# Optimization experiments

Hardware: AMD Instinct MI355X
Metric: run time of the kernel (lower is better)

The kernel has to match this reference:

```python
import jax, jax.numpy as jnp
import numpy as np

N, B, T, D = 4, 4, 512, 512
H, DK, DV = 8, 64, 64
LN_EPS = 1e-5


def setup_inputs() -> dict:
    key = jax.random.key(0)
    ks = jax.random.split(key, 5)
    s = 1.0 / np.sqrt(D)
    return {
        "x": jax.random.normal(ks[0], (N, B, T, D), jnp.float32),
        "Wq": jax.random.normal(ks[1], (D, H * DK), jnp.float32) * s,
        "bq": jnp.zeros((H * DK,), jnp.float32),
        "Wk": jax.random.normal(ks[2], (D, H * DK), jnp.float32) * s,
        "bk": jnp.zeros((H * DK,), jnp.float32),
        "Wv": jax.random.normal(ks[3], (D, H * DV), jnp.float32) * s,
        "bv": jnp.zeros((H * DV,), jnp.float32),
        "Wo": jax.random.normal(ks[4], (H * DV, D), jnp.float32) * (1.0 / np.sqrt(H * DV)),
        "bo": jnp.zeros((D,), jnp.float32),
        "gamma": jnp.ones((D,), jnp.float32),
        "beta": jnp.zeros((D,), jnp.float32),
    }


def reference(x, Wq, bq, Wk, bk, Wv, bv, Wo, bo, gamma, beta):
    # x: [N, B, T, D] -- N variables, each [B, T, D]
    n = x.shape[0]
    # Project once per variable (the torch code redundantly recomputes K/V per query var).
    q = (x @ Wq + bq).reshape(n, B, T, H, DK).transpose(0, 1, 3, 2, 4)  # [N,B,H,T,DK]
    k = (x @ Wk + bk).reshape(n, B, T, H, DK).transpose(0, 1, 3, 2, 4)  # [N,B,H,T,DK]
    v = (x @ Wv + bv).reshape(n, B, T, H, DV).transpose(0, 1, 3, 2, 4)  # [N,B,H,T,DV]
    # All-pairs attention: softmax over keys of EACH key-variable separately.
    scores = jnp.einsum('qbhtk,cbhsk->qcbhts', q, k) / np.sqrt(DK)  # [Nq,Nc,B,H,T,T]
    attn = jax.nn.softmax(scores, axis=-1)
    ctx = jnp.einsum('qcbhts,cbhsv->qcbhtv', attn, v)  # [Nq,Nc,B,H,T,DV]
    ctx = ctx.transpose(0, 1, 2, 4, 3, 5).reshape(n, n, B, T, H * DV)
    out = ctx @ Wo + bo                     # per-pair output projection
    out = out.sum(axis=1) / n               # average over key variables -> [N,B,T,D]
    res = x + out
    mu = res.mean(axis=-1, keepdims=True)
    var = res.var(axis=-1, keepdims=True)
    y = (res - mu) / jnp.sqrt(var + LN_EPS) * gamma + beta
    return y
```

## Files before the change

kernel.cpp:

```cpp
#include <hip/hip_runtime.h>


typedef __bf16 bf16x8 __attribute__((ext_vector_type(8)));
typedef __bf16 bf16x4 __attribute__((ext_vector_type(4)));
typedef short shortx4 __attribute__((ext_vector_type(4)));
typedef float floatx4 __attribute__((ext_vector_type(4)));
typedef float floatx16 __attribute__((ext_vector_type(16)));
typedef unsigned short ushortx8 __attribute__((ext_vector_type(8)));

static __device__ __forceinline__ unsigned short f2bf(float f) {
  union { __bf16 h; unsigned short u; } c; c.h = (__bf16)f; return c.u;
}

__global__ __launch_bounds__(256) void cvt_f32_bf16(
    const float* __restrict__ in, unsigned short* __restrict__ out)
{
  const int i = blockIdx.x * 256 + threadIdx.x;
  const float4 a = ((const float4*)in)[i * 2];
  const float4 b = ((const float4*)in)[i * 2 + 1];
  ushortx8 o;
  o[0] = f2bf(a.x); o[1] = f2bf(a.y); o[2] = f2bf(a.z); o[3] = f2bf(a.w);
  o[4] = f2bf(b.x); o[5] = f2bf(b.y); o[6] = f2bf(b.z); o[7] = f2bf(b.w);
  *(ushortx8*)(out + (size_t)i * 8) = o;
}

__global__ __launch_bounds__(256) void transpose_w(
    const float* __restrict__ W0, const float* __restrict__ W1,
    const float* __restrict__ W2, const float* __restrict__ W3,
    unsigned short* __restrict__ T0, unsigned short* __restrict__ T1,
    unsigned short* __restrict__ T2, unsigned short* __restrict__ T3)
{
  __shared__ unsigned short lds[64][65];
  const float* W; unsigned short* T;
  if (blockIdx.z == 0)      { W = W0; T = T0; }
  else if (blockIdx.z == 1) { W = W1; T = T1; }
  else if (blockIdx.z == 2) { W = W2; T = T2; }
  else                      { W = W3; T = T3; }
  const int xx = threadIdx.x;
  const int yy = threadIdx.y;
  const int k0 = blockIdx.x * 64, n0 = blockIdx.y * 64;
#pragma unroll
  for (int i = 0; i < 16; ++i) {
    const int row = yy * 16 + i;
    lds[row][xx] = f2bf(W[(size_t)(k0 + row) * 512 + n0 + xx]);
  }
  __syncthreads();
#pragma unroll
  for (int i = 0; i < 16; ++i) {
    const int nr = yy * 16 + i;
    T[(size_t)(n0 + nr) * 512 + k0 + xx] = lds[xx][nr];
  }
}

template<int MODE>
__global__ __launch_bounds__(256) void gemm64(
    const unsigned short* __restrict__ A,
    const unsigned short* __restrict__ BT,
    const float* __restrict__ bias,
    void* __restrict__ Cout, float scale)
{
  __shared__ __align__(16) unsigned short lA[64][72];
  __shared__ __align__(16) unsigned short lB[64][72];
  const int tid  = threadIdx.x;
  const int wv   = tid >> 6, lane = tid & 63;
  const int quad = lane >> 4, l16 = lane & 15;
  const int m0 = blockIdx.x * 64, n0 = blockIdx.y * 64;
  floatx4 acc[4] = {};
  const int lrow = tid >> 2, lc0 = (tid & 3) * 16;

  for (int kc = 0; kc < 512; kc += 64) {
    __syncthreads();
    const unsigned short* as = A + (size_t)(m0 + lrow) * 512 + kc + lc0;
    *(bf16x8*)&lA[lrow][lc0]     = *(const bf16x8*)as;
    *(bf16x8*)&lA[lrow][lc0 + 8] = *(const bf16x8*)(as + 8);
    const unsigned short* bs = BT + (size_t)(n0 + lrow) * 512 + kc + lc0;
    *(bf16x8*)&lB[lrow][lc0]     = *(const bf16x8*)bs;
    *(bf16x8*)&lB[lrow][lc0 + 8] = *(const bf16x8*)(bs + 8);
    __syncthreads();
    bf16x8 a0 = *(const bf16x8*)&lA[wv * 16 + l16][quad * 8];
    bf16x8 a1 = *(const bf16x8*)&lA[wv * 16 + l16][32 + quad * 8];
#pragma unroll
    for (int ni = 0; ni < 4; ++ni) {
      bf16x8 b0 = *(const bf16x8*)&lB[ni * 16 + l16][quad * 8];
      bf16x8 b1 = *(const bf16x8*)&lB[ni * 16 + l16][32 + quad * 8];
      acc[ni] = __builtin_amdgcn_mfma_f32_16x16x32_bf16(a0, b0, acc[ni], 0, 0, 0);
      acc[ni] = __builtin_amdgcn_mfma_f32_16x16x32_bf16(a1, b1, acc[ni], 0, 0, 0);
    }
  }

  const int mbase = m0 + wv * 16 + quad * 4;
  float bv4[4];
  if (MODE != 2) {
#pragma unroll
    for (int ni = 0; ni < 4; ++ni) bv4[ni] = bias[n0 + ni * 16 + l16];
  }
#pragma unroll
  for (int ni = 0; ni < 4; ++ni) {
    const int n = n0 + ni * 16 + l16;
#pragma unroll
    for (int r = 0; r < 4; ++r) {
      const int m = mbase + r;
      float v = acc[ni][r];
      if (MODE != 2) v = (v + bv4[ni]) * scale;
      if (MODE == 0) {
        const int nb = m >> 9, t = m & 511, hh = n >> 6, dk = n & 63;
        ((unsigned short*)Cout)[((size_t)(nb * 8 + hh) * 512 + t) * 64 + dk] = f2bf(v);
      } else if (MODE == 1) {
        const int nb = m >> 9, t = m & 511, hh = n >> 6, dk = n & 63;
        ((unsigned short*)Cout)[((size_t)(nb * 8 + hh) * 64 + dk) * 512 + t] = f2bf(v);
      } else {
        ((float*)Cout)[(size_t)m * 512 + n] = v;
      }
    }
  }
}

__global__ __launch_bounds__(256) void flash_kernel(
    const unsigned short* __restrict__ Q,
    const unsigned short* __restrict__ K,
    const unsigned short* __restrict__ VT,
    unsigned short* __restrict__ CTX)
{
  __shared__ __align__(16) unsigned short lK[2][64][72];
  __shared__ __align__(16) unsigned short lV[2][64][68];
  const int tid  = threadIdx.x;
  const int wv   = tid >> 6, lane = tid & 63;
  const int l32  = lane & 31, u = lane >> 5;

  const int lin  = blockIdx.y * 4 + blockIdx.x;
  const int xcd  = lin & 7, slot = lin >> 3;
  const int nbh  = xcd * 16 + (slot >> 2);
  const int t0   = (slot & 3) * 128;
  const int h = nbh & 7, nb = nbh >> 3, b = nb & 3;

  const unsigned short* qbase = Q + ((size_t)nbh * 512 + (t0 + wv * 32 + l32)) * 64;
  bf16x8 qf[4];
#pragma unroll
  for (int c16 = 0; c16 < 4; ++c16)
    qf[c16] = *(const bf16x8*)(qbase + c16 * 16 + u * 8);

  const int srow = tid >> 2, sc0 = (tid & 3) * 16;
  const unsigned short *kptr, *vptr;
  auto setptr = [&](int it) {
    const int c = it >> 3, s0 = (it & 7) * 64;
    const size_t kvbh = (size_t)((c * 4 + b) * 8 + h);
    kptr = K  + kvbh * (512 * 64) + (size_t)(s0 + srow) * 64 + sc0;
    vptr = VT + kvbh * (64 * 512) + (size_t)srow * 512 + s0 + sc0;
  };
  bf16x8 rk0, rk1, rv0, rv1;
  auto loadregs = [&]() {
    rk0 = *(const bf16x8*)kptr; rk1 = *(const bf16x8*)(kptr + 8);
    rv0 = *(const bf16x8*)vptr; rv1 = *(const bf16x8*)(vptr + 8);
  };
  auto writebuf = [&](int p) {
    *(bf16x8*)&lK[p][srow][sc0]     = rk0;
    *(bf16x8*)&lK[p][srow][sc0 + 8] = rk1;
    union { bf16x8 v8; bf16x4 v4[2]; } c0, c1;
    c0.v8 = rv0; c1.v8 = rv1;
    *(bf16x4*)&lV[p][srow][sc0]      = c0.v4[0];
    *(bf16x4*)&lV[p][srow][sc0 + 4]  = c0.v4[1];
    *(bf16x4*)&lV[p][srow][sc0 + 8]  = c1.v4[0];
    *(bf16x4*)&lV[p][srow][sc0 + 12] = c1.v4[1];
  };

  setptr(0); loadregs();
  writebuf(0);
  setptr(1); loadregs();
  __syncthreads();

  floatx16 ofin0 = {}, ofin1 = {};
  floatx16 oc0, oc1;
  float lacc;

  for (int it = 0; it < 32; ++it) {
    const int cur = it & 1;
    const int st = it & 7;
    if (st == 0) { oc0 = floatx16{}; oc1 = floatx16{}; lacc = 0.f; }

    if (it < 31) writebuf(cur ^ 1);
    if (it < 30) { setptr(it + 2); loadregs(); }

    floatx16 sacc0 = {}, sacc1 = {};
#pragma unroll
    for (int c16 = 0; c16 < 4; ++c16) {
      bf16x8 ak0 = *(const bf16x8*)&lK[cur][l32][c16 * 16 + u * 8];
      bf16x8 ak1 = *(const bf16x8*)&lK[cur][32 + l32][c16 * 16 + u * 8];
      sacc0 = __builtin_amdgcn_mfma_f32_32x32x16_bf16(ak0, qf[c16], sacc0, 0, 0, 0);
      sacc1 = __builtin_amdgcn_mfma_f32_32x32x16_bf16(ak1, qf[c16], sacc1, 0, 0, 0);
    }

#pragma unroll
    for (int sb = 0; sb < 2; ++sb) {
      const floatx16& sa = sb ? sacc1 : sacc0;
#pragma unroll
      for (int c8 = 0; c8 < 4; ++c8) {
        float e0 = __expf(sa[4 * c8 + 0] - 12.0f);
        float e1 = __expf(sa[4 * c8 + 1] - 12.0f);
        float e2 = __expf(sa[4 * c8 + 2] - 12.0f);
        float e3 = __expf(sa[4 * c8 + 3] - 12.0f);
        lacc += (e0 + e1) + (e2 + e3);
        shortx4 pf;
        pf[0] = (short)f2bf(e0); pf[1] = (short)f2bf(e1);
        pf[2] = (short)f2bf(e2); pf[3] = (short)f2bf(e3);
        const int sloc = sb * 32 + c8 * 8 + u * 4;
        shortx4 vf0 = *(const shortx4*)&lV[cur][l32][sloc];
        shortx4 vf1 = *(const shortx4*)&lV[cur][32 + l32][sloc];
        oc0 = __builtin_amdgcn_mfma_f32_32x32x8bf16_1k(pf, vf0, oc0, 0, 0, 0);
        oc1 = __builtin_amdgcn_mfma_f32_32x32x8bf16_1k(pf, vf1, oc1, 0, 0, 0);
      }
    }

    if (st == 7) {
      float s = lacc;
      s += __shfl_xor(s, 32);
      const float inv = 1.0f / s;
#pragma unroll
      for (int r = 0; r < 16; ++r) {
        const int trow = (r & 3) + 8 * (r >> 2) + 4 * u;
        const float invr = __shfl(inv, trow);
        ofin0[r] += oc0[r] * invr;
        ofin1[r] += oc1[r] * invr;
      }
    }
    __syncthreads();
  }

  const int mbase = nb * 512 + t0 + wv * 32;
#pragma unroll
  for (int r = 0; r < 16; ++r) {
    const int trow = (r & 3) + 8 * (r >> 2) + 4 * u;
    const size_t rowoff = (size_t)(mbase + trow) * 512 + h * 64;
    CTX[rowoff + l32]      = f2bf(ofin0[r]);
    CTX[rowoff + 32 + l32] = f2bf(ofin1[r]);
  }
}

__global__ __launch_bounds__(256) void ln_kernel(
    const float* __restrict__ x, const float* __restrict__ tmp,
    const float* __restrict__ bo, const float* __restrict__ gamma,
    const float* __restrict__ beta, float* __restrict__ out)
{
  const int row = blockIdx.x;
  const int t = threadIdx.x;
  const size_t base = (size_t)row * 512;
  const float r0 = x[base + t]       + 0.25f * tmp[base + t]       + bo[t];
  const float r1 = x[base + t + 256] + 0.25f * tmp[base + t + 256] + bo[t + 256];
  float s = r0 + r1, sq = r0 * r0 + r1 * r1;
#pragma unroll
  for (int off = 1; off < 64; off <<= 1) {
    s  += __shfl_xor(s, off);
    sq += __shfl_xor(sq, off);
  }
  __shared__ float ls[4], lq[4];
  const int wv = t >> 6, lane = t & 63;
  if (lane == 0) { ls[wv] = s; lq[wv] = sq; }
  __syncthreads();
  s  = ls[0] + ls[1] + ls[2] + ls[3];
  sq = lq[0] + lq[1] + lq[2] + lq[3];
  const float mu  = s * (1.0f / 512.0f);
  const float var = sq * (1.0f / 512.0f) - mu * mu;
  const float inv = rsqrtf(var + 1e-5f);
  out[base + t]       = (r0 - mu) * inv * gamma[t]       + beta[t];
  out[base + t + 256] = (r1 - mu) * inv * gamma[t + 256] + beta[t + 256];
}

extern "C" void kernel_launch(void* const* d_in, const int* in_sizes, int n_in,
                              void* d_out, int out_size, void* d_ws, size_t ws_size,
                              hipStream_t stream) {
  const float* x     = (const float*)d_in[0];
  const float* Wq    = (const float*)d_in[1];
  const float* bq    = (const float*)d_in[2];
  const float* Wk    = (const float*)d_in[3];
  const float* bk    = (const float*)d_in[4];
  const float* Wv    = (const float*)d_in[5];
  const float* bv    = (const float*)d_in[6];
  const float* Wo    = (const float*)d_in[7];
  const float* bo    = (const float*)d_in[8];
  const float* gamma = (const float*)d_in[9];
  const float* beta  = (const float*)d_in[10];
  float* out = (float*)d_out;

  char* w = (char*)d_ws;
  unsigned short* x_bf  = (unsigned short*)(w);
  unsigned short* q_bf  = (unsigned short*)(w + (size_t)8  * 1024 * 1024);
  unsigned short* k_bf  = (unsigned short*)(w + (size_t)16 * 1024 * 1024);
  unsigned short* vt_bf = (unsigned short*)(w + (size_t)24 * 1024 * 1024);
  unsigned short* ctx   = (unsigned short*)(w + (size_t)32 * 1024 * 1024);
  unsigned short* wqT   = (unsigned short*)(w + (size_t)40 * 1024 * 1024);
  unsigned short* wkT   = wqT + 262144;
  unsigned short* wvT   = wkT + 262144;
  unsigned short* woT   = wvT + 262144;
  float* tmp            = (float*)(w);

  cvt_f32_bf16<<<2048, 256, 0, stream>>>(x, x_bf);
  transpose_w<<<dim3(8, 8, 4), dim3(64, 4), 0, stream>>>(Wq, Wk, Wv, Wo, wqT, wkT, wvT, woT);
  gemm64<0><<<dim3(128, 8), 256, 0, stream>>>(x_bf, wqT, bq, q_bf, 0.125f);
  gemm64<0><<<dim3(128, 8), 256, 0, stream>>>(x_bf, wkT, bk, k_bf, 1.0f);
  gemm64<1><<<dim3(128, 8), 256, 0, stream>>>(x_bf, wvT, bv, vt_bf, 1.0f);
  flash_kernel<<<dim3(4, 128), 256, 0, stream>>>(q_bf, k_bf, vt_bf, ctx);
  gemm64<2><<<dim3(128, 8), 256, 0, stream>>>(ctx, woT, nullptr, tmp, 1.0f);
  ln_kernel<<<8192, 256, 0, stream>>>(x, tmp, bo, gamma, beta, out);
}
```

Baseline: 204.8 us.

## Split attention over key-variable groups, fuse QKV GEMMs and input conversion

The flash kernel now splits the four key variables into two groups, which doubles the number of blocks. Each group writes a partial context, and a new reduce kernel sums the two. The separate fp32-to-bf16 conversion of x is folded into a single merged QKV GEMM launch that covers all three projections. The softmax moves to exp2, with the log2(e) factor folded into the Q scale and the constant shift used to initialise the score accumulators. In exchange, this adds an extra bf16 partial-sum round trip through memory and an extra kernel launch.

Measured after the change: 214.3 us. 1.05x slower.

```diff
diff --git a/kernel.cpp b/kernel.cpp
--- a/kernel.cpp
+++ b/kernel.cpp
@@ -11,18 +11,12 @@
 static __device__ __forceinline__ unsigned short f2bf(float f) {
   union { __bf16 h; unsigned short u; } c; c.h = (__bf16)f; return c.u;
 }
-
-__global__ __launch_bounds__(256) void cvt_f32_bf16(
-    const float* __restrict__ in, unsigned short* __restrict__ out)
-{
-  const int i = blockIdx.x * 256 + threadIdx.x;
-  const float4 a = ((const float4*)in)[i * 2];
-  const float4 b = ((const float4*)in)[i * 2 + 1];
-  ushortx8 o;
-  o[0] = f2bf(a.x); o[1] = f2bf(a.y); o[2] = f2bf(a.z); o[3] = f2bf(a.w);
-  o[4] = f2bf(b.x); o[5] = f2bf(b.y); o[6] = f2bf(b.z); o[7] = f2bf(b.w);
-  *(ushortx8*)(out + (size_t)i * 8) = o;
-}
+static __device__ __forceinline__ float bf2f(unsigned short u) {
+  union { unsigned u32; float f; } c; c.u32 = ((unsigned)u) << 16; return c.f;
+}
+
+#define QSCALE 0.18033688011112042f
+#define SHIFT2 (-17.312340489609306f)
 
 __global__ __launch_bounds__(256) void transpose_w(
     const float* __restrict__ W0, const float* __restrict__ W1,
@@ -52,12 +46,78 @@
   }
 }
 
-template<int MODE>
-__global__ __launch_bounds__(256) void gemm64(
+__global__ __launch_bounds__(256) void gemm_qkv(
+    const float* __restrict__ X,
+    const unsigned short* __restrict__ BT,
+    const float* __restrict__ bq, const float* __restrict__ bk,
+    const float* __restrict__ bv,
+    unsigned short* __restrict__ Qo, unsigned short* __restrict__ Ko,
+    unsigned short* __restrict__ Vo)
+{
+  __shared__ __align__(16) unsigned short lA[64][72];
+  __shared__ __align__(16) unsigned short lB[64][72];
+  const int tid  = threadIdx.x;
+  const int wv   = tid >> 6, lane = tid & 63;
+  const int quad = lane >> 4, l16 = lane & 15;
+  const int m0 = blockIdx.x * 64, n0g = blockIdx.y * 64;
+  const int sel = n0g >> 9;
+  const int n0  = n0g & 511;
+  const float* bias = (sel == 0) ? bq : (sel == 1) ? bk : bv;
+  unsigned short* outp = (sel == 0) ? Qo : (sel == 1) ? Ko : Vo;
+  const float scale = (sel == 0) ? QSCALE : 1.0f;
+  floatx4 acc[4] = {};
+  const int lrow = tid >> 2, lc0 = (tid & 3) * 16;
+
+  for (int kc = 0; kc < 512; kc += 64) {
+    __syncthreads();
+    const float* as = X + (size_t)(m0 + lrow) * 512 + kc + lc0;
+    float4 a0 = *(const float4*)as,       a1 = *(const float4*)(as + 4);
+    float4 a2 = *(const float4*)(as + 8), a3 = *(const float4*)(as + 12);
+    ushortx8 p0, p1;
+    p0[0]=f2bf(a0.x); p0[1]=f2bf(a0.y); p0[2]=f2bf(a0.z); p0[3]=f2bf(a0.w);
+    p0[4]=f2bf(a1.x); p0[5]=f2bf(a1.y); p0[6]=f2bf(a1.z); p0[7]=f2bf(a1.w);
+    p1[0]=f2bf(a2.x); p1[1]=f2bf(a2.y); p1[2]=f2bf(a2.z); p1[3]=f2bf(a2.w);
+    p1[4]=f2bf(a3.x); p1[5]=f2bf(a3.y); p1[6]=f2bf(a3.z); p1[7]=f2bf(a3.w);
+    *(ushortx8*)&lA[lrow][lc0]     = p0;
+    *(ushortx8*)&lA[lrow][lc0 + 8] = p1;
+    const unsigned short* bs = BT + (size_t)(n0g + lrow) * 512 + kc + lc0;
+    *(bf16x8*)&lB[lrow][lc0]     = *(const bf16x8*)bs;
+    *(bf16x8*)&lB[lrow][lc0 + 8] = *(const bf16x8*)(bs + 8);
+    __syncthreads();
+    bf16x8 a0f = *(const bf16x8*)&lA[wv * 16 + l16][quad * 8];
+    bf16x8 a1f = *(const bf16x8*)&lA[wv * 16 + l16][32 + quad * 8];
+#pragma unroll
+    for (int ni = 0; ni < 4; ++ni) {
+      bf16x8 b0 = *(const bf16x8*)&lB[ni * 16 + l16][quad * 8];
+      bf16x8 b1 = *(const bf16x8*)&lB[ni * 16 + l16][32 + quad * 8];
+      acc[ni] = __builtin_amdgcn_mfma_f32_16x16x32_bf16(a0f, b0, acc[ni], 0, 0, 0);
+      acc[ni] = __builtin_amdgcn_mfma_f32_16x16x32_bf16(a1f, b1, acc[ni], 0, 0, 0);
+    }
+  }
+
+  const int mbase = m0 + wv * 16 + quad * 4;
+#pragma unroll
+  for (int ni = 0; ni < 4; ++ni) {
+    const int nl = n0 + ni * 16 + l16;
+    const float bvv = bias[nl];
+    const int hh = nl >> 6, dk = nl & 63;
+#pragma unroll
+    for (int r = 0; r < 4; ++r) {
+      const int m = mbase + r;
+      const int nb = m >> 9, t = m & 511;
+      const float v = (acc[ni][r] + bvv) * scale;
+      if (sel == 2)
+        outp[((size_t)(nb * 8 + hh) * 64 + dk) * 512 + t] = f2bf(v);
+      else
+        outp[((size_t)(nb * 8 + hh) * 512 + t) * 64 + dk] = f2bf(v);
+    }
+  }
+}
+
+__global__ __launch_bounds__(256) void gemm_out(
     const unsigned short* __restrict__ A,
     const unsigned short* __restrict__ BT,
-    const float* __restrict__ bias,
-    void* __restrict__ Cout, float scale)
+    float* __restrict__ Cout)
 {
   __shared__ __align__(16) unsigned short lA[64][72];
   __shared__ __align__(16) unsigned short lB[64][72];
@@ -87,31 +147,13 @@
       acc[ni] = __builtin_amdgcn_mfma_f32_16x16x32_bf16(a1, b1, acc[ni], 0, 0, 0);
     }
   }
-
   const int mbase = m0 + wv * 16 + quad * 4;
-  float bv4[4];
-  if (MODE != 2) {
-#pragma unroll
-    for (int ni = 0; ni < 4; ++ni) bv4[ni] = bias[n0 + ni * 16 + l16];
-  }
 #pragma unroll
   for (int ni = 0; ni < 4; ++ni) {
     const int n = n0 + ni * 16 + l16;
 #pragma unroll
-    for (int r = 0; r < 4; ++r) {
-      const int m = mbase + r;
-      float v = acc[ni][r];
-      if (MODE != 2) v = (v + bv4[ni]) * scale;
-      if (MODE == 0) {
-        const int nb = m >> 9, t = m & 511, hh = n >> 6, dk = n & 63;
-        ((unsigned short*)Cout)[((size_t)(nb * 8 + hh) * 512 + t) * 64 + dk] = f2bf(v);
-      } else if (MODE == 1) {
-        const int nb = m >> 9, t = m & 511, hh = n >> 6, dk = n & 63;
-        ((unsigned short*)Cout)[((size_t)(nb * 8 + hh) * 64 + dk) * 512 + t] = f2bf(v);
-      } else {
-        ((float*)Cout)[(size_t)m * 512 + n] = v;
-      }
-    }
+    for (int r = 0; r < 4; ++r)
+      Cout[(size_t)(mbase + r) * 512 + n] = acc[ni][r];
   }
 }
 
@@ -119,7 +161,7 @@
     const unsigned short* __restrict__ Q,
     const unsigned short* __restrict__ K,
     const unsigned short* __restrict__ VT,
-    unsigned short* __restrict__ CTX)
+    unsigned short* __restrict__ CTX2)
 {
   __shared__ __align__(16) unsigned short lK[2][64][72];
   __shared__ __align__(16) unsigned short lV[2][64][68];
@@ -127,10 +169,12 @@
   const int wv   = tid >> 6, lane = tid & 63;
   const int l32  = lane & 31, u = lane >> 5;
 
-  const int lin  = blockIdx.y * 4 + blockIdx.x;
+  const int lin  = blockIdx.x;
   const int xcd  = lin & 7, slot = lin >> 3;
-  const int nbh  = xcd * 16 + (slot >> 2);
-  const int t0   = (slot & 3) * 128;
+  const int tile = slot & 3;
+  const int nbh  = xcd * 16 + ((slot >> 2) & 15);
+  const int cg   = slot >> 6;
+  const int t0   = tile * 128;
   const int h = nbh & 7, nb = nbh >> 3, b = nb & 3;
 
   const unsigned short* qbase = Q + ((size_t)nbh * 512 + (t0 + wv * 32 + l32)) * 64;
@@ -142,7 +186,7 @@
   const int srow = tid >> 2, sc0 = (tid & 3) * 16;
   const unsigned short *kptr, *vptr;
   auto setptr = [&](int it) {
-    const int c = it >> 3, s0 = (it & 7) * 64;
+    const int c = cg * 2 + (it >> 3), s0 = (it & 7) * 64;
     const size_t kvbh = (size_t)((c * 4 + b) * 8 + h);
     kptr = K  + kvbh * (512 * 64) + (size_t)(s0 + srow) * 64 + sc0;
     vptr = VT + kvbh * (64 * 512) + (size_t)srow * 512 + s0 + sc0;
@@ -172,15 +216,17 @@
   floatx16 oc0, oc1;
   float lacc;
 
-  for (int it = 0; it < 32; ++it) {
+  for (int it = 0; it < 16; ++it) {
     const int cur = it & 1;
     const int st = it & 7;
     if (st == 0) { oc0 = floatx16{}; oc1 = floatx16{}; lacc = 0.f; }
 
-    if (it < 31) writebuf(cur ^ 1);
-    if (it < 30) { setptr(it + 2); loadregs(); }
-
-    floatx16 sacc0 = {}, sacc1 = {};
+    if (it < 15) writebuf(cur ^ 1);
+    if (it < 14) { setptr(it + 2); loadregs(); }
+
+    floatx16 sacc0, sacc1;
+#pragma unroll
+    for (int r = 0; r < 16; ++r) { sacc0[r] = SHIFT2; sacc1[r] = SHIFT2; }
 #pragma unroll
     for (int c16 = 0; c16 < 4; ++c16) {
       bf16x8 ak0 = *(const bf16x8*)&lK[cur][l32][c16 * 16 + u * 8];
@@ -194,10 +240,10 @@
       const floatx16& sa = sb ? sacc1 : sacc0;
 #pragma unroll
       for (int c8 = 0; c8 < 4; ++c8) {
-        float e0 = __expf(sa[4 * c8 + 0] - 12.0f);
-        float e1 = __expf(sa[4 * c8 + 1] - 12.0f);
-        float e2 = __expf(sa[4 * c8 + 2] - 12.0f);
-        float e3 = __expf(sa[4 * c8 + 3] - 12.0f);
+        float e0 = __builtin_amdgcn_exp2f(sa[4 * c8 + 0]);
+        float e1 = __builtin_amdgcn_exp2f(sa[4 * c8 + 1]);
+        float e2 = __builtin_amdgcn_exp2f(sa[4 * c8 + 2]);
+        float e3 = __builtin_amdgcn_exp2f(sa[4 * c8 + 3]);
         lacc += (e0 + e1) + (e2 + e3);
         shortx4 pf;
         pf[0] = (short)f2bf(e0); pf[1] = (short)f2bf(e1);
@@ -225,14 +271,28 @@
     __syncthreads();
   }
 
+  unsigned short* outp = CTX2 + (size_t)cg * (8192 * 512);
   const int mbase = nb * 512 + t0 + wv * 32;
 #pragma unroll
   for (int r = 0; r < 16; ++r) {
     const int trow = (r & 3) + 8 * (r >> 2) + 4 * u;
     const size_t rowoff = (size_t)(mbase + trow) * 512 + h * 64;
-    CTX[rowoff + l32]      = f2bf(ofin0[r]);
-    CTX[rowoff + 32 + l32] = f2bf(ofin1[r]);
-  }
+    outp[rowoff + l32]      = f2bf(ofin0[r]);
+    outp[rowoff + 32 + l32] = f2bf(ofin1[r]);
+  }
+}
+
+__global__ __launch_bounds__(256) void reduce2(
+    const unsigned short* __restrict__ A, const unsigned short* __restrict__ B,
+    unsigned short* __restrict__ O)
+{
+  const size_t i = ((size_t)blockIdx.x * 256 + threadIdx.x) * 8;
+  ushortx8 a = *(const ushortx8*)(A + i);
+  ushortx8 b = *(const ushortx8*)(B + i);
+  ushortx8 o;
+#pragma unroll
+  for (int j = 0; j < 8; ++j) o[j] = f2bf(bf2f(a[j]) + bf2f(b[j]));
+  *(ushortx8*)(O + i) = o;
 }
 
 __global__ __launch_bounds__(256) void ln_kernel(
@@ -281,23 +341,21 @@
   float* out = (float*)d_out;
 
   char* w = (char*)d_ws;
-  unsigned short* x_bf  = (unsigned short*)(w);
-  unsigned short* q_bf  = (unsigned short*)(w + (size_t)8  * 1024 * 1024);
-  unsigned short* k_bf  = (unsigned short*)(w + (size_t)16 * 1024 * 1024);
-  unsigned short* vt_bf = (unsigned short*)(w + (size_t)24 * 1024 * 1024);
-  unsigned short* ctx   = (unsigned short*)(w + (size_t)32 * 1024 * 1024);
-  unsigned short* wqT   = (unsigned short*)(w + (size_t)40 * 1024 * 1024);
-  unsigned short* wkT   = wqT + 262144;
-  unsigned short* wvT   = wkT + 262144;
-  unsigned short* woT   = wvT + 262144;
-  float* tmp            = (float*)(w);
-
-  cvt_f32_bf16<<<2048, 256, 0, stream>>>(x, x_bf);
-  transpose_w<<<dim3(8, 8, 4), dim3(64, 4), 0, stream>>>(Wq, Wk, Wv, Wo, wqT, wkT, wvT, woT);
-  gemm64<0><<<dim3(128, 8), 256, 0, stream>>>(x_bf, wqT, bq, q_bf, 0.125f);
-  gemm64<0><<<dim3(128, 8), 256, 0, stream>>>(x_bf, wkT, bk, k_bf, 1.0f);
-  gemm64<1><<<dim3(128, 8), 256, 0, stream>>>(x_bf, wvT, bv, vt_bf, 1.0f);
-  flash_kernel<<<dim3(4, 128), 256, 0, stream>>>(q_bf, k_bf, vt_bf, ctx);
-  gemm64<2><<<dim3(128, 8), 256, 0, stream>>>(ctx, woT, nullptr, tmp, 1.0f);
+  unsigned short* q_bf  = (unsigned short*)(w);
+  unsigned short* k_bf  = (unsigned short*)(w + (size_t)8  * 1024 * 1024);
+  unsigned short* vt_bf = (unsigned short*)(w + (size_t)16 * 1024 * 1024);
+  unsigned short* ctx2  = (unsigned short*)(w + (size_t)24 * 1024 * 1024);
+  unsigned short* wqkvT = (unsigned short*)(w + (size_t)40 * 1024 * 1024);
+  unsigned short* woT   = wqkvT + 786432;
+  unsigned short* ctx   = (unsigned short*)(w);
+  float* tmp            = (float*)(w + (size_t)8 * 1024 * 1024);
+
+  transpose_w<<<dim3(8, 8, 4), dim3(64, 4), 0, stream>>>(
+      Wq, Wk, Wv, Wo, wqkvT, wqkvT + 262144, wqkvT + 524288, woT);
+  gemm_qkv<<<dim3(128, 24), 256, 0, stream>>>(x, wqkvT, bq, bk, bv,
+                                              q_bf, k_bf, vt_bf);
+  flash_kernel<<<1024, 256, 0, stream>>>(q_bf, k_bf, vt_bf, ctx2);
+  reduce2<<<2048, 256, 0, stream>>>(ctx2, ctx2 + (size_t)8192 * 512, ctx);
+  gemm_out<<<dim3(128, 8), 256, 0, stream>>>(ctx, woT, tmp);
   ln_kernel<<<8192, 256, 0, stream>>>(x, tmp, bo, gamma, beta, out);
 }
```
